# Kernel optimization log

Hardware: AMD Instinct MI355X
Metric: run time of the kernel (lower is better)

Reference implementation:

```python
import jax, jax.numpy as jnp
import numpy as np

EPS = 1e-12  # torch F.normalize eps

def _l2norm(t):
    # F.normalize(t, p=2, dim=1): divide by clamped L2 norm
    n = jnp.sqrt(jnp.sum(t * t, axis=1, keepdims=True))
    return t / jnp.maximum(n, EPS)


def setup_inputs() -> dict:
    key = jax.random.key(0)
    k1, k2, k3 = jax.random.split(key, 3)
    N, K, D = 262144, 512, 64
    inputs = jax.random.normal(k1, (N, D), dtype=jnp.float32)
    labels = jax.random.randint(k2, (N,), 0, K, dtype=jnp.int64)
    embedding = jax.random.normal(k3, (K, D), dtype=jnp.float32)
    return {"inputs": inputs, "labels": labels, "embedding": embedding}


def reference(inputs, labels, embedding):
    K, D = embedding.shape
    flat = inputs.reshape(-1, D)  # [N, D]
    # cosine similarity: [N, K]
    distances = _l2norm(flat) @ _l2norm(embedding).T
    encoding_indices = jnp.argmax(distances, axis=1)  # [N]
    encodings = jax.nn.one_hot(encoding_indices, K, dtype=flat.dtype)  # [N, K]
    # quantize lookup via one-hot matmul (as in original)
    quantized = (encodings @ embedding).reshape(inputs.shape)
    # labeled branch: closs = mean(1 - distances[i, labels[i]])
    picked = jnp.take_along_axis(distances, labels[:, None], axis=1)[:, 0]
    loss = jnp.mean(1.0 - picked)
    # straight-through estimator
    quantized = inputs + jax.lax.stop_gradient(quantized - inputs)
    perplexity = jnp.array(1, dtype=jnp.int32)
    return (loss, quantized, perplexity, encodings, encoding_indices[:, None])
```

## Files before the change

### kernel.cpp

```cpp
#include <hip/hip_runtime.h>
#include <math.h>

#define N_ROWS 262144
#define KCODES 512
#define DIM 64
#define BLOCK 256
#define ROWS_PER_BLOCK 128
#define KTILE 64
#define NSTAGES (KCODES / KTILE)
#define LDS_ROW 72
#define PLANE_STRIDE (KTILE * LDS_ROW)

typedef __attribute__((ext_vector_type(8))) short short8;
typedef __attribute__((ext_vector_type(4))) float f4;

static const size_t OFF_LOSS = 0;
static const size_t OFF_Q    = 1;
static const size_t OFF_PERP = 1 + (size_t)N_ROWS * DIM;
static const size_t OFF_ENC  = OFF_PERP + 1;
static const size_t OFF_IDX  = OFF_ENC + (size_t)N_ROWS * KCODES;

__device__ __forceinline__ unsigned short bf16rne(float f) {
    unsigned int u = __float_as_uint(f);
    u = (u + 0x7fffu + ((u >> 16) & 1u)) >> 16;
    return (unsigned short)u;
}
__device__ __forceinline__ float bf16tof(unsigned short h) {
    return __uint_as_float(((unsigned int)h) << 16);
}

__global__ __launch_bounds__(64) void vq_prep(const float* __restrict__ emb,
                                              unsigned short* __restrict__ ph,
                                              unsigned short* __restrict__ pm,
                                              unsigned short* __restrict__ pl,
                                              float* __restrict__ out_loss,
                                              float* __restrict__ out_perp) {
    int k = blockIdx.x;
    int d = threadIdx.x;
    float v = emb[k * DIM + d];
    float s = v * v;
    #pragma unroll
    for (int off = 32; off > 0; off >>= 1) s += __shfl_xor(s, off, 64);
    float vn = v / fmaxf(sqrtf(s), 1e-12f);
    unsigned short h = bf16rne(vn);
    float r = vn - bf16tof(h);
    unsigned short m = bf16rne(r);
    r = r - bf16tof(m);
    unsigned short l = bf16rne(r);
    ph[k * DIM + d] = h;
    pm[k * DIM + d] = m;
    pl[k * DIM + d] = l;
    if (k == 0 && d == 0) { *out_loss = 0.0f; *out_perp = 1.0f; }
}

#define MFMA(A, B, C) C = __builtin_amdgcn_mfma_f32_16x16x32_bf16(A, B, C, 0, 0, 0)

__global__ __launch_bounds__(BLOCK, 3) void vq_main(const float* __restrict__ x,
                                                    const int* __restrict__ labels,
                                                    const float* __restrict__ emb,
                                                    const unsigned short* __restrict__ ph,
                                                    const unsigned short* __restrict__ pm,
                                                    const unsigned short* __restrict__ pl,
                                                    float* __restrict__ out_loss,
                                                    float* __restrict__ out_q,
                                                    float* __restrict__ out_enc,
                                                    float* __restrict__ out_idx) {
    const int tid   = threadIdx.x;
    const int wv    = tid >> 6;
    const int lane  = tid & 63;
    const int q     = lane >> 4;
    const int c     = lane & 15;
    const int wbase = blockIdx.x * ROWS_PER_BLOCK + wv * 32;

    __shared__ __align__(16) unsigned short sE[3 * PLANE_STRIDE];
    __shared__ int   sIdx[4][32];
    __shared__ float sPick[4][32];
    __shared__ float sInv[4][32];
    __shared__ float sLoss[4];

    float inv_nx[2];
    short8 Ah[2][2], Am[2][2], Al[2][2];
    #pragma unroll
    for (int t = 0; t < 2; ++t) {
        float xv[16];
        const float* xp = x + (size_t)(wbase + t * 16 + c) * DIM + q * 8;
        #pragma unroll
        for (int s = 0; s < 2; ++s) {
            float4 lo = *(const float4*)(xp + s * 32);
            float4 hi = *(const float4*)(xp + s * 32 + 4);
            xv[s * 8 + 0] = lo.x; xv[s * 8 + 1] = lo.y;
            xv[s * 8 + 2] = lo.z; xv[s * 8 + 3] = lo.w;
            xv[s * 8 + 4] = hi.x; xv[s * 8 + 5] = hi.y;
            xv[s * 8 + 6] = hi.z; xv[s * 8 + 7] = hi.w;
        }
        float s2 = 0.f;
        #pragma unroll
        for (int j = 0; j < 16; ++j) s2 = fmaf(xv[j], xv[j], s2);
        s2 += __shfl_xor(s2, 16, 64);
        s2 += __shfl_xor(s2, 32, 64);
        inv_nx[t] = 1.0f / fmaxf(sqrtf(s2), 1e-12f);
        #pragma unroll
        for (int s = 0; s < 2; ++s)
            #pragma unroll
            for (int j = 0; j < 8; ++j) {
                float v = xv[s * 8 + j];
                unsigned short h = bf16rne(v);
                float r = v - bf16tof(h);
                unsigned short m = bf16rne(r);
                r = r - bf16tof(m);
                unsigned short l = bf16rne(r);
                Ah[t][s][j] = (short)h;
                Am[t][s][j] = (short)m;
                Al[t][s][j] = (short)l;
            }
    }

    int   lbl[2][4];
    float best[2][4], pick[2][4];
    int   bidx[2][4];
    #pragma unroll
    for (int t = 0; t < 2; ++t)
        #pragma unroll
        for (int r = 0; r < 4; ++r) {
            lbl[t][r]  = labels[wbase + t * 16 + q * 4 + r];
            best[t][r] = -3.4e38f;
            bidx[t][r] = 0;
            pick[t][r] = 0.f;
        }

    for (int st = 0; st < NSTAGES; ++st) {
        __syncthreads();
        #pragma unroll
        for (int i = 0; i < 2; ++i) {
            int ch = tid + i * BLOCK;
            int code = ch >> 3, part = ch & 7;
            int dst = code * LDS_ROW + part * 8;
            int src = st * (KTILE * DIM) + ch * 8;
            *(float4*)&sE[dst]                    = *(const float4*)(ph + src);
            *(float4*)&sE[PLANE_STRIDE + dst]     = *(const float4*)(pm + src);
            *(float4*)&sE[2 * PLANE_STRIDE + dst] = *(const float4*)(pl + src);
        }
        __syncthreads();

        #pragma unroll 2
        for (int sub = 0; sub < KTILE / 16; ++sub) {
            const unsigned short* bp = &sE[(sub * 16 + c) * LDS_ROW + q * 8];
            short8 Bh0 = *(const short8*)(bp);
            short8 Bh1 = *(const short8*)(bp + 32);
            short8 Bm0 = *(const short8*)(bp + PLANE_STRIDE);
            short8 Bm1 = *(const short8*)(bp + PLANE_STRIDE + 32);
            short8 Bl0 = *(const short8*)(bp + 2 * PLANE_STRIDE);
            short8 Bl1 = *(const short8*)(bp + 2 * PLANE_STRIDE + 32);

            f4 acc0 = {0.f, 0.f, 0.f, 0.f};
            f4 acc1 = {0.f, 0.f, 0.f, 0.f};
            MFMA(Ah[0][0], Bh0, acc0);  MFMA(Ah[1][0], Bh0, acc1);
            MFMA(Ah[0][1], Bh1, acc0);  MFMA(Ah[1][1], Bh1, acc1);
            MFMA(Ah[0][0], Bm0, acc0);  MFMA(Ah[1][0], Bm0, acc1);
            MFMA(Ah[0][1], Bm1, acc0);  MFMA(Ah[1][1], Bm1, acc1);
            MFMA(Am[0][0], Bh0, acc0);  MFMA(Am[1][0], Bh0, acc1);
            MFMA(Am[0][1], Bh1, acc0);  MFMA(Am[1][1], Bh1, acc1);
            MFMA(Ah[0][0], Bl0, acc0);  MFMA(Ah[1][0], Bl0, acc1);
            MFMA(Ah[0][1], Bl1, acc0);  MFMA(Ah[1][1], Bl1, acc1);
            MFMA(Al[0][0], Bh0, acc0);  MFMA(Al[1][0], Bh0, acc1);
            MFMA(Al[0][1], Bh1, acc0);  MFMA(Al[1][1], Bh1, acc1);
            MFMA(Am[0][0], Bm0, acc0);  MFMA(Am[1][0], Bm0, acc1);
            MFMA(Am[0][1], Bm1, acc0);  MFMA(Am[1][1], Bm1, acc1);

            const int code = st * KTILE + sub * 16 + c;
            #pragma unroll
            for (int r = 0; r < 4; ++r) {
                float d0 = acc0[r];
                if (d0 > best[0][r]) { best[0][r] = d0; bidx[0][r] = code; }
                if (code == lbl[0][r]) pick[0][r] = d0;
                float d1 = acc1[r];
                if (d1 > best[1][r]) { best[1][r] = d1; bidx[1][r] = code; }
                if (code == lbl[1][r]) pick[1][r] = d1;
            }
        }
    }

    #pragma unroll
    for (int t = 0; t < 2; ++t)
        #pragma unroll
        for (int r = 0; r < 4; ++r) {
            float b = best[t][r]; int i = bidx[t][r]; float p = pick[t][r];
            #pragma unroll
            for (int m = 1; m < 16; m <<= 1) {
                float ob = __shfl_xor(b, m, 64);
                int   oi = __shfl_xor(i, m, 64);
                p += __shfl_xor(p, m, 64);
                if (ob > b || (ob == b && oi < i)) { b = ob; i = oi; }
            }
            bidx[t][r] = i; pick[t][r] = p;
        }

    if (c == 0) {
        #pragma unroll
        for (int t = 0; t < 2; ++t)
            #pragma unroll
            for (int r = 0; r < 4; ++r) {
                int rl = t * 16 + q * 4 + r;
                sIdx[wv][rl]  = bidx[t][r];
                sPick[wv][rl] = pick[t][r];
            }
    }
    if (q == 0) { sInv[wv][c] = inv_nx[0]; sInv[wv][16 + c] = inv_nx[1]; }
    __syncthreads();

    {
        const int col0 = lane * 4, col1 = 256 + lane * 4;
        for (int r = 0; r < 32; ++r) {
            int bi = sIdx[wv][r];
            float* base = out_enc + (size_t)(wbase + r) * KCODES;
            f4 v0 = { bi == col0     ? 1.f : 0.f,
                      bi == col0 + 1 ? 1.f : 0.f,
                      bi == col0 + 2 ? 1.f : 0.f,
                      bi == col0 + 3 ? 1.f : 0.f };
            __builtin_nontemporal_store(v0, (f4*)(base + col0));
            f4 v1 = { bi == col1     ? 1.f : 0.f,
                      bi == col1 + 1 ? 1.f : 0.f,
                      bi == col1 + 2 ? 1.f : 0.f,
                      bi == col1 + 3 ? 1.f : 0.f };
            __builtin_nontemporal_store(v1, (f4*)(base + col1));
        }
    }

    #pragma unroll
    for (int i = 0; i < 8; ++i) {
        int r  = i * 4 + q;
        int bi = sIdx[wv][r];
        f4 v = ((const f4*)(emb + (size_t)bi * DIM))[c];
        __builtin_nontemporal_store(v, ((f4*)(out_q + (size_t)(wbase + r) * DIM)) + c);
    }

    if (lane < 32) out_idx[wbase + lane] = (float)sIdx[wv][lane];

    float lv = 0.f;
    if (lane < 32)
        lv = (1.0f - sPick[wv][lane] * sInv[wv][lane]) * (1.0f / (float)N_ROWS);
    #pragma unroll
    for (int m = 1; m < 64; m <<= 1) lv += __shfl_xor(lv, m, 64);
    if (lane == 0) sLoss[wv] = lv;
    __syncthreads();
    if (tid == 0)
        atomicAdd(out_loss, sLoss[0] + sLoss[1] + sLoss[2] + sLoss[3]);
}

extern "C" void kernel_launch(void* const* d_in, const int* in_sizes, int n_in,
                              void* d_out, int out_size, void* d_ws, size_t ws_size,
                              hipStream_t stream) {
    const float* x      = (const float*)d_in[0];
    const int*   labels = (const int*)d_in[1];
    const float* emb    = (const float*)d_in[2];
    float* out = (float*)d_out;
    unsigned short* ph = (unsigned short*)d_ws;
    unsigned short* pm = ph + (size_t)KCODES * DIM;
    unsigned short* pl = pm + (size_t)KCODES * DIM;

    hipLaunchKernelGGL(vq_prep, dim3(KCODES), dim3(64), 0, stream,
                       emb, ph, pm, pl, out + OFF_LOSS, out + OFF_PERP);
    hipLaunchKernelGGL(vq_main, dim3(N_ROWS / ROWS_PER_BLOCK), dim3(BLOCK), 0, stream,
                       x, labels, emb, ph, pm, pl,
                       out + OFF_LOSS, out + OFF_Q, out + OFF_ENC, out + OFF_IDX);
}
```

Baseline: 703.0 us.

## Drop LDS staging, read fragment-packed codebook from global, overlap one-hot zeroing with MFMA

```diff
diff --git a/kernel.cpp b/kernel.cpp
--- a/kernel.cpp
+++ b/kernel.cpp
@@ -6,10 +6,7 @@
 #define DIM 64
 #define BLOCK 256
 #define ROWS_PER_BLOCK 128
-#define KTILE 64
-#define NSTAGES (KCODES / KTILE)
-#define LDS_ROW 72
-#define PLANE_STRIDE (KTILE * LDS_ROW)
+#define CODE_STRIDE 192
 
 typedef __attribute__((ext_vector_type(8))) short short8;
 typedef __attribute__((ext_vector_type(4))) float f4;
@@ -30,9 +27,7 @@
 }
 
 __global__ __launch_bounds__(64) void vq_prep(const float* __restrict__ emb,
-                                              unsigned short* __restrict__ ph,
-                                              unsigned short* __restrict__ pm,
-                                              unsigned short* __restrict__ pl,
+                                              unsigned short* __restrict__ pe,
                                               float* __restrict__ out_loss,
                                               float* __restrict__ out_perp) {
     int k = blockIdx.x;
@@ -47,9 +42,11 @@
     unsigned short m = bf16rne(r);
     r = r - bf16tof(m);
     unsigned short l = bf16rne(r);
-    ph[k * DIM + d] = h;
-    pm[k * DIM + d] = m;
-    pl[k * DIM + d] = l;
+    int ss = d >> 5, qq = (d >> 3) & 3, j = d & 7;
+    unsigned short* base = pe + k * CODE_STRIDE + qq * 48;
+    base[ss * 8 + j]      = h;
+    base[16 + ss * 8 + j] = m;
+    base[32 + ss * 8 + j] = l;
     if (k == 0 && d == 0) { *out_loss = 0.0f; *out_perp = 1.0f; }
 }
 
@@ -58,9 +55,7 @@
 __global__ __launch_bounds__(BLOCK, 3) void vq_main(const float* __restrict__ x,
                                                     const int* __restrict__ labels,
                                                     const float* __restrict__ emb,
-                                                    const unsigned short* __restrict__ ph,
-                                                    const unsigned short* __restrict__ pm,
-                                                    const unsigned short* __restrict__ pl,
+                                                    const unsigned short* __restrict__ pe,
                                                     float* __restrict__ out_loss,
                                                     float* __restrict__ out_q,
                                                     float* __restrict__ out_enc,
@@ -71,12 +66,6 @@
     const int q     = lane >> 4;
     const int c     = lane & 15;
     const int wbase = blockIdx.x * ROWS_PER_BLOCK + wv * 32;
-
-    __shared__ __align__(16) unsigned short sE[3 * PLANE_STRIDE];
-    __shared__ int   sIdx[4][32];
-    __shared__ float sPick[4][32];
-    __shared__ float sInv[4][32];
-    __shared__ float sLoss[4];
 
     float inv_nx[2];
     short8 Ah[2][2], Am[2][2], Al[2][2];
@@ -128,57 +117,51 @@
             pick[t][r] = 0.f;
         }
 
-    for (int st = 0; st < NSTAGES; ++st) {
-        __syncthreads();
-        #pragma unroll
-        for (int i = 0; i < 2; ++i) {
-            int ch = tid + i * BLOCK;
-            int code = ch >> 3, part = ch & 7;
-            int dst = code * LDS_ROW + part * 8;
-            int src = st * (KTILE * DIM) + ch * 8;
-            *(float4*)&sE[dst]                    = *(const float4*)(ph + src);
-            *(float4*)&sE[PLANE_STRIDE + dst]     = *(const float4*)(pm + src);
-            *(float4*)&sE[2 * PLANE_STRIDE + dst] = *(const float4*)(pl + src);
-        }
-        __syncthreads();
-
-        #pragma unroll 2
-        for (int sub = 0; sub < KTILE / 16; ++sub) {
-            const unsigned short* bp = &sE[(sub * 16 + c) * LDS_ROW + q * 8];
-            short8 Bh0 = *(const short8*)(bp);
-            short8 Bh1 = *(const short8*)(bp + 32);
-            short8 Bm0 = *(const short8*)(bp + PLANE_STRIDE);
-            short8 Bm1 = *(const short8*)(bp + PLANE_STRIDE + 32);
-            short8 Bl0 = *(const short8*)(bp + 2 * PLANE_STRIDE);
-            short8 Bl1 = *(const short8*)(bp + 2 * PLANE_STRIDE + 32);
-
-            f4 acc0 = {0.f, 0.f, 0.f, 0.f};
-            f4 acc1 = {0.f, 0.f, 0.f, 0.f};
-            MFMA(Ah[0][0], Bh0, acc0);  MFMA(Ah[1][0], Bh0, acc1);
-            MFMA(Ah[0][1], Bh1, acc0);  MFMA(Ah[1][1], Bh1, acc1);
-            MFMA(Ah[0][0], Bm0, acc0);  MFMA(Ah[1][0], Bm0, acc1);
-            MFMA(Ah[0][1], Bm1, acc0);  MFMA(Ah[1][1], Bm1, acc1);
-            MFMA(Am[0][0], Bh0, acc0);  MFMA(Am[1][0], Bh0, acc1);
-            MFMA(Am[0][1], Bh1, acc0);  MFMA(Am[1][1], Bh1, acc1);
-            MFMA(Ah[0][0], Bl0, acc0);  MFMA(Ah[1][0], Bl0, acc1);
-            MFMA(Ah[0][1], Bl1, acc0);  MFMA(Ah[1][1], Bl1, acc1);
-            MFMA(Al[0][0], Bh0, acc0);  MFMA(Al[1][0], Bh0, acc1);
-            MFMA(Al[0][1], Bh1, acc0);  MFMA(Al[1][1], Bh1, acc1);
-            MFMA(Am[0][0], Bm0, acc0);  MFMA(Am[1][0], Bm0, acc1);
-            MFMA(Am[0][1], Bm1, acc0);  MFMA(Am[1][1], Bm1, acc1);
-
-            const int code = st * KTILE + sub * 16 + c;
-            #pragma unroll
-            for (int r = 0; r < 4; ++r) {
-                float d0 = acc0[r];
-                if (d0 > best[0][r]) { best[0][r] = d0; bidx[0][r] = code; }
-                if (code == lbl[0][r]) pick[0][r] = d0;
-                float d1 = acc1[r];
-                if (d1 > best[1][r]) { best[1][r] = d1; bidx[1][r] = code; }
-                if (code == lbl[1][r]) pick[1][r] = d1;
-            }
+    #pragma unroll 2
+    for (int st = 0; st < KCODES / 16; ++st) {
+        const unsigned short* bp = pe + (size_t)(st * 16 + c) * CODE_STRIDE + q * 48;
+        short8 Bh0 = *(const short8*)(bp);
+        short8 Bh1 = *(const short8*)(bp + 8);
+        short8 Bm0 = *(const short8*)(bp + 16);
+        short8 Bm1 = *(const short8*)(bp + 24);
+        short8 Bl0 = *(const short8*)(bp + 32);
+        short8 Bl1 = *(const short8*)(bp + 40);
+
+        {
+            float* zb = out_enc + (size_t)(wbase + st) * KCODES;
+            f4 z = {0.f, 0.f, 0.f, 0.f};
+            __builtin_nontemporal_store(z, (f4*)(zb + lane * 4));
+            __builtin_nontemporal_store(z, (f4*)(zb + 256 + lane * 4));
+        }
+
+        f4 acc0 = {0.f, 0.f, 0.f, 0.f};
+        f4 acc1 = {0.f, 0.f, 0.f, 0.f};
+        MFMA(Ah[0][0], Bh0, acc0);  MFMA(Ah[1][0], Bh0, acc1);
+        MFMA(Ah[0][1], Bh1, acc0);  MFMA(Ah[1][1], Bh1, acc1);
+        MFMA(Ah[0][0], Bm0, acc0);  MFMA(Ah[1][0], Bm0, acc1);
+        MFMA(Ah[0][1], Bm1, acc0);  MFMA(Ah[1][1], Bm1, acc1);
+        MFMA(Am[0][0], Bh0, acc0);  MFMA(Am[1][0], Bh0, acc1);
+        MFMA(Am[0][1], Bh1, acc0);  MFMA(Am[1][1], Bh1, acc1);
+        MFMA(Ah[0][0], Bl0, acc0);  MFMA(Ah[1][0], Bl0, acc1);
+        MFMA(Ah[0][1], Bl1, acc0);  MFMA(Ah[1][1], Bl1, acc1);
+        MFMA(Al[0][0], Bh0, acc0);  MFMA(Al[1][0], Bh0, acc1);
+        MFMA(Al[0][1], Bh1, acc0);  MFMA(Al[1][1], Bh1, acc1);
+        MFMA(Am[0][0], Bm0, acc0);  MFMA(Am[1][0], Bm0, acc1);
+        MFMA(Am[0][1], Bm1, acc0);  MFMA(Am[1][1], Bm1, acc1);
+
+        const int code = st * 16 + c;
+        #pragma unroll
+        for (int r = 0; r < 4; ++r) {
+            float d0 = acc0[r];
+            if (d0 > best[0][r]) { best[0][r] = d0; bidx[0][r] = code; }
+            if (code == lbl[0][r]) pick[0][r] = d0;
+            float d1 = acc1[r];
+            if (d1 > best[1][r]) { best[1][r] = d1; bidx[1][r] = code; }
+            if (code == lbl[1][r]) pick[1][r] = d1;
         }
     }
+
+    asm volatile("s_waitcnt vmcnt(0)" ::: "memory");
 
     #pragma unroll
     for (int t = 0; t < 2; ++t)
@@ -200,51 +183,33 @@
         for (int t = 0; t < 2; ++t)
             #pragma unroll
             for (int r = 0; r < 4; ++r) {
-                int rl = t * 16 + q * 4 + r;
-                sIdx[wv][rl]  = bidx[t][r];
-                sPick[wv][rl] = pick[t][r];
+                int row = wbase + t * 16 + q * 4 + r;
+                out_enc[(size_t)row * KCODES + bidx[t][r]] = 1.0f;
+                out_idx[row] = (float)bidx[t][r];
             }
     }
-    if (q == 0) { sInv[wv][c] = inv_nx[0]; sInv[wv][16 + c] = inv_nx[1]; }
-    __syncthreads();
-
-    {
-        const int col0 = lane * 4, col1 = 256 + lane * 4;
-        for (int r = 0; r < 32; ++r) {
-            int bi = sIdx[wv][r];
-            float* base = out_enc + (size_t)(wbase + r) * KCODES;
-            f4 v0 = { bi == col0     ? 1.f : 0.f,
-                      bi == col0 + 1 ? 1.f : 0.f,
-                      bi == col0 + 2 ? 1.f : 0.f,
-                      bi == col0 + 3 ? 1.f : 0.f };
-            __builtin_nontemporal_store(v0, (f4*)(base + col0));
-            f4 v1 = { bi == col1     ? 1.f : 0.f,
-                      bi == col1 + 1 ? 1.f : 0.f,
-                      bi == col1 + 2 ? 1.f : 0.f,
-                      bi == col1 + 3 ? 1.f : 0.f };
-            __builtin_nontemporal_store(v1, (f4*)(base + col1));
-        }
-    }
-
-    #pragma unroll
-    for (int i = 0; i < 8; ++i) {
-        int r  = i * 4 + q;
-        int bi = sIdx[wv][r];
-        f4 v = ((const f4*)(emb + (size_t)bi * DIM))[c];
-        __builtin_nontemporal_store(v, ((f4*)(out_q + (size_t)(wbase + r) * DIM)) + c);
-    }
-
-    if (lane < 32) out_idx[wbase + lane] = (float)sIdx[wv][lane];
+
+    #pragma unroll
+    for (int t = 0; t < 2; ++t)
+        #pragma unroll
+        for (int r = 0; r < 4; ++r) {
+            int row = wbase + t * 16 + q * 4 + r;
+            f4 v = ((const f4*)(emb + (size_t)bidx[t][r] * DIM))[c];
+            __builtin_nontemporal_store(v, ((f4*)(out_q + (size_t)row * DIM)) + c);
+        }
 
     float lv = 0.f;
-    if (lane < 32)
-        lv = (1.0f - sPick[wv][lane] * sInv[wv][lane]) * (1.0f / (float)N_ROWS);
+    #pragma unroll
+    for (int t = 0; t < 2; ++t)
+        #pragma unroll
+        for (int r = 0; r < 4; ++r) {
+            float invv = __shfl(inv_nx[t], q * 4 + r, 64);
+            lv += (1.0f - pick[t][r] * invv);
+        }
+    lv *= 1.0f / ((float)N_ROWS * 16.0f);
     #pragma unroll
     for (int m = 1; m < 64; m <<= 1) lv += __shfl_xor(lv, m, 64);
-    if (lane == 0) sLoss[wv] = lv;
-    __syncthreads();
-    if (tid == 0)
-        atomicAdd(out_loss, sLoss[0] + sLoss[1] + sLoss[2] + sLoss[3]);
+    if (lane == 0) atomicAdd(out_loss, lv);
 }
 
 extern "C" void kernel_launch(void* const* d_in, const int* in_sizes, int n_in,
@@ -254,13 +219,11 @@
     const int*   labels = (const int*)d_in[1];
     const float* emb    = (const float*)d_in[2];
     float* out = (float*)d_out;
-    unsigned short* ph = (unsigned short*)d_ws;
-    unsigned short* pm = ph + (size_t)KCODES * DIM;
-    unsigned short* pl = pm + (size_t)KCODES * DIM;
+    unsigned short* pe = (unsigned short*)d_ws;
 
     hipLaunchKernelGGL(vq_prep, dim3(KCODES), dim3(64), 0, stream,
-                       emb, ph, pm, pl, out + OFF_LOSS, out + OFF_PERP);
+                       emb, pe, out + OFF_LOSS, out + OFF_PERP);
     hipLaunchKernelGGL(vq_main, dim3(N_ROWS / ROWS_PER_BLOCK), dim3(BLOCK), 0, stream,
-                       x, labels, emb, ph, pm, pl,
+                       x, labels, emb, pe,
                        out + OFF_LOSS, out + OFF_Q, out + OFF_ENC, out + OFF_IDX);
 }
```

Result: slower. 788.9 us (+12.2%).

## Zero one-hot rows during MFMA loop and scatter ones per row

Applied to the files above, without the earlier changes.

```diff
diff --git a/kernel.cpp b/kernel.cpp
--- a/kernel.cpp
+++ b/kernel.cpp
@@ -73,10 +73,6 @@
     const int wbase = blockIdx.x * ROWS_PER_BLOCK + wv * 32;
 
     __shared__ __align__(16) unsigned short sE[3 * PLANE_STRIDE];
-    __shared__ int   sIdx[4][32];
-    __shared__ float sPick[4][32];
-    __shared__ float sInv[4][32];
-    __shared__ float sLoss[4];
 
     float inv_nx[2];
     short8 Ah[2][2], Am[2][2], Al[2][2];
@@ -151,6 +147,14 @@
             short8 Bm1 = *(const short8*)(bp + PLANE_STRIDE + 32);
             short8 Bl0 = *(const short8*)(bp + 2 * PLANE_STRIDE);
             short8 Bl1 = *(const short8*)(bp + 2 * PLANE_STRIDE + 32);
+
+            {
+                int g = st * (KTILE / 16) + sub;
+                float* zb = out_enc + (size_t)(wbase + g) * KCODES;
+                f4 z = {0.f, 0.f, 0.f, 0.f};
+                __builtin_nontemporal_store(z, (f4*)(zb + lane * 4));
+                __builtin_nontemporal_store(z, (f4*)(zb + 256 + lane * 4));
+            }
 
             f4 acc0 = {0.f, 0.f, 0.f, 0.f};
             f4 acc1 = {0.f, 0.f, 0.f, 0.f};
@@ -180,6 +184,8 @@
         }
     }
 
+    asm volatile("s_waitcnt vmcnt(0)" ::: "memory");
+
     #pragma unroll
     for (int t = 0; t < 2; ++t)
         #pragma unroll
@@ -200,51 +206,33 @@
         for (int t = 0; t < 2; ++t)
             #pragma unroll
             for (int r = 0; r < 4; ++r) {
-                int rl = t * 16 + q * 4 + r;
-                sIdx[wv][rl]  = bidx[t][r];
-                sPick[wv][rl] = pick[t][r];
+                int row = wbase + t * 16 + q * 4 + r;
+                out_enc[(size_t)row * KCODES + bidx[t][r]] = 1.0f;
+                out_idx[row] = (float)bidx[t][r];
             }
     }
-    if (q == 0) { sInv[wv][c] = inv_nx[0]; sInv[wv][16 + c] = inv_nx[1]; }
-    __syncthreads();
-
-    {
-        const int col0 = lane * 4, col1 = 256 + lane * 4;
-        for (int r = 0; r < 32; ++r) {
-            int bi = sIdx[wv][r];
-            float* base = out_enc + (size_t)(wbase + r) * KCODES;
-            f4 v0 = { bi == col0     ? 1.f : 0.f,
-                      bi == col0 + 1 ? 1.f : 0.f,
-                      bi == col0 + 2 ? 1.f : 0.f,
-                      bi == col0 + 3 ? 1.f : 0.f };
-            __builtin_nontemporal_store(v0, (f4*)(base + col0));
-            f4 v1 = { bi == col1     ? 1.f : 0.f,
-                      bi == col1 + 1 ? 1.f : 0.f,
-                      bi == col1 + 2 ? 1.f : 0.f,
-                      bi == col1 + 3 ? 1.f : 0.f };
-            __builtin_nontemporal_store(v1, (f4*)(base + col1));
-        }
-    }
-
-    #pragma unroll
-    for (int i = 0; i < 8; ++i) {
-        int r  = i * 4 + q;
-        int bi = sIdx[wv][r];
-        f4 v = ((const f4*)(emb + (size_t)bi * DIM))[c];
-        __builtin_nontemporal_store(v, ((f4*)(out_q + (size_t)(wbase + r) * DIM)) + c);
-    }
-
-    if (lane < 32) out_idx[wbase + lane] = (float)sIdx[wv][lane];
+
+    #pragma unroll
+    for (int t = 0; t < 2; ++t)
+        #pragma unroll
+        for (int r = 0; r < 4; ++r) {
+            int row = wbase + t * 16 + q * 4 + r;
+            f4 v = ((const f4*)(emb + (size_t)bidx[t][r] * DIM))[c];
+            __builtin_nontemporal_store(v, ((f4*)(out_q + (size_t)row * DIM)) + c);
+        }
 
     float lv = 0.f;
-    if (lane < 32)
-        lv = (1.0f - sPick[wv][lane] * sInv[wv][lane]) * (1.0f / (float)N_ROWS);
+    #pragma unroll
+    for (int t = 0; t < 2; ++t)
+        #pragma unroll
+        for (int r = 0; r < 4; ++r) {
+            float invv = __shfl(inv_nx[t], q * 4 + r, 64);
+            lv += (1.0f - pick[t][r] * invv);
+        }
+    lv *= 1.0f / ((float)N_ROWS * 16.0f);
     #pragma unroll
     for (int m = 1; m < 64; m <<= 1) lv += __shfl_xor(lv, m, 64);
-    if (lane == 0) sLoss[wv] = lv;
-    __syncthreads();
-    if (tid == 0)
-        atomicAdd(out_loss, sLoss[0] + sLoss[1] + sLoss[2] + sLoss[3]);
+    if (lane == 0) atomicAdd(out_loss, lv);
 }
 
 extern "C" void kernel_launch(void* const* d_in, const int* in_sizes, int n_in,
```

New measurement: 737.4 us. +4.9%, slower.
